# Performance work log

Hardware: AMD Instinct MI355X
Metric: run time of the kernel (lower is better)

Reference implementation:

```python
import jax, jax.numpy as jnp
import numpy as np
from jax import lax

EPS = 1e-5
NUM_CLASSES = 133


def conv2d(x, w, stride, pad, b=None):
    # x: [N,C,H,W], w: [O,I,kh,kw]
    out = lax.conv_general_dilated(x, w, (stride, stride), ((pad, pad), (pad, pad)),
                                   dimension_numbers=('NCHW', 'OIHW', 'NCHW'))
    if b is not None:
        out = out + b[None, :, None, None]
    return out


def cbn(x, y, embed_w, C):
    # ConditionalBatchNorm2d in training mode: batch stats (biased var), affine from embedding
    mean = x.mean(axis=(0, 2, 3), keepdims=True)
    var = x.var(axis=(0, 2, 3), keepdims=True)
    xn = (x - mean) * lax.rsqrt(var + EPS)
    gb = embed_w[y]                      # [O, 2C]
    gamma, beta = gb[:, :C], gb[:, C:]
    return gamma[:, :, None, None] * xn + beta[:, :, None, None]


def lrelu(x):
    return jnp.where(x >= 0, x, 0.2 * x)


def clstm_layer(x_seq, w, b, hidden_dim):
    # x_seq: [T, B, Cin, 16, 16] -> (all h: [T,B,hid,16,16], last h: [B,hid,16,16])
    B = x_seq.shape[1]
    h0 = jnp.zeros((B, hidden_dim, 16, 16), x_seq.dtype)

    def step(carry, x):
        h, c = carry
        cc = conv2d(jnp.concatenate([x, h], axis=1), w, 1, 2, b)  # k=5, pad=2
        i, f, o, g = jnp.split(cc, 4, axis=1)
        c = jax.nn.sigmoid(f) * c + jax.nn.sigmoid(i) * jnp.tanh(g)
        h = jax.nn.sigmoid(o) * jnp.tanh(c)
        return (h, c), h

    (h, _), hs = lax.scan(step, (h0, h0), x_seq)
    return hs, h


def setup_inputs() -> dict:
    key = jax.random.key(0)
    ks = jax.random.split(key, 24)
    O, C_in, H = 8, 512, 254
    B, T = 4, 2
    d = {}
    d['h'] = jax.random.normal(ks[0], (O, C_in, H, H), jnp.float32)
    d['objs'] = jax.random.randint(ks[1], (O,), 0, NUM_CLASSES)
    d['obj_to_img'] = jnp.repeat(jnp.arange(B), T)  # sorted, equal-sized groups

    def w(k, shape):
        fan_in = shape[1] * shape[2] * shape[3]
        return jax.random.normal(k, shape, jnp.float32) / np.sqrt(fan_in)

    def embed(k, C):
        g = 1.0 + 0.02 * jax.random.normal(k, (NUM_CLASSES, C), jnp.float32)
        return jnp.concatenate([g, jnp.zeros((NUM_CLASSES, C), jnp.float32)], axis=1)

    d['c1_w'] = w(ks[2], (32, 512, 1, 1))
    d['c2_w'] = w(ks[3], (64, 32, 4, 4))
    d['c3_w'] = w(ks[4], (128, 64, 4, 4))
    d['c4_w'] = w(ks[5], (256, 128, 4, 4))
    d['c5_w'] = w(ks[6], (512, 256, 4, 4))
    d['e1'] = embed(ks[7], 32)
    d['e2'] = embed(ks[8], 64)
    d['e3'] = embed(ks[9], 128)
    d['e4'] = embed(ks[10], 256)
    d['e5'] = embed(ks[11], 512)
    # ConvLSTM layers: hidden [128, 64, 64], kernel 5x5, input_dim 512
    d['lw0'] = w(ks[12], (4 * 128, 512 + 128, 5, 5))
    d['lb0'] = jnp.zeros((4 * 128,), jnp.float32)
    d['lw1'] = w(ks[13], (4 * 64, 128 + 64, 5, 5))
    d['lb1'] = jnp.zeros((4 * 64,), jnp.float32)
    d['lw2'] = w(ks[14], (4 * 64, 64 + 64, 5, 5))
    d['lb2'] = jnp.zeros((4 * 64,), jnp.float32)
    return d


def reference(objs, obj_to_img, h, c1_w, c2_w, c3_w, c4_w, c5_w,
              e1, e2, e3, e4, e5, lw0, lb0, lw1, lb1, lw2, lb2):
    x = lrelu(cbn(conv2d(h, c1_w, 1, 1), objs, e1, 32))    # [O,32,256,256]
    x = lrelu(cbn(conv2d(x, c2_w, 2, 1), objs, e2, 64))    # [O,64,128,128]
    x = lrelu(cbn(conv2d(x, c3_w, 2, 1), objs, e3, 128))   # [O,128,64,64]
    x = cbn(conv2d(x, c4_w, 2, 1), objs, e4, 256)          # no activation after bn4 (as in source)
    x = cbn(conv2d(x, c5_w, 2, 1), objs, e5, 512)          # [O,512,16,16], no activation after bn5

    # Group ragged per-image object sequences. The torch loop groups consecutive
    # equal obj_to_img ids; with equal group sizes this is a static reshape.
    o2i = np.asarray(obj_to_img)
    B = int(o2i.max()) + 1
    O = x.shape[0]
    T = O // B
    assert B * T == O, 'reference assumes equal-sized, sorted object groups'
    seq = x.reshape(B, T, 512, 16, 16).transpose(1, 0, 2, 3, 4)  # [T,B,512,16,16]

    hs, _ = clstm_layer(seq, lw0, lb0, 128)
    hs, _ = clstm_layer(hs, lw1, lb1, 64)
    _, h_last = clstm_layer(hs, lw2, lb2, 64)
    return h_last  # [B,64,16,16]
```

## Files before the change

kernel.cpp:

```cpp
#include <hip/hip_runtime.h>
#include <math.h>

#define LEAK 0.2f

typedef __attribute__((ext_vector_type(8))) short bf16x8;
typedef __attribute__((ext_vector_type(4))) float f32x4;

__device__ __forceinline__ unsigned short f2bf(float f) {
  unsigned u = __float_as_uint(f);
  u += 0x7FFFu + ((u >> 16) & 1u);
  return (unsigned short)(u >> 16);
}
__device__ __forceinline__ unsigned pack2(float a, float b) {
  return (unsigned)f2bf(a) | ((unsigned)f2bf(b) << 16);
}

#define MFMA16(a, b, c) __builtin_amdgcn_mfma_f32_16x16x32_bf16(a, b, c, 0, 0, 0)

__global__ __launch_bounds__(256) void wprepT_kernel(
    const float* c1w, const float* c2w, const float* c3w, const float* c4w,
    const float* c5w, const float* lw0, const float* lw1, const float* lw2,
    unsigned short* wb1, unsigned short* wb2, unsigned short* wb3,
    unsigned short* wb4, unsigned short* wb5, unsigned short* wbf0,
    unsigned short* wbf1, unsigned short* wbf2)
{
  __shared__ float lds[256 * 26];
  const int tid = threadIdx.x;
  int b = blockIdx.x;

  const float* src;
  unsigned short* dst;
  int T, OC, base;
  if (b < 8)         { src = c2w; dst = wb2;  T = 16; OC = 2048;   base = b * 256; }
  else if (b < 40)   { src = c3w; dst = wb3;  T = 16; OC = 8192;   base = (b - 8) * 256; }
  else if (b < 168)  { src = c4w; dst = wb4;  T = 16; OC = 32768;  base = (b - 40) * 256; }
  else if (b < 680)  { src = c5w; dst = wb5;  T = 16; OC = 131072; base = (b - 168) * 256; }
  else if (b < 872)  { src = lw1; dst = wbf1; T = 25; OC = 49152;  base = (b - 680) * 256; }
  else if (b < 1000) { src = lw2; dst = wbf2; T = 25; OC = 32768;  base = (b - 872) * 256; }
  else if (b < 2280) { src = lw0; dst = wbf0; T = 25; OC = 327680; base = (b - 1000) * 256; }
  else {
    int i = (b - 2280) * 256 + tid;
    int o = i >> 9, c = i & 511;
    wb1[(((c >> 5) * 32) + o) * 32 + (c & 31)] = f2bf(c1w[i]);
    return;
  }

  const float* sp = src + (size_t)base * T;
  for (int e = tid; e < 256 * T; e += 256) {
    int oc = e / T, tap = e - oc * T;
    lds[oc * 26 + tap] = sp[e];
  }
  __syncthreads();
  for (int tap = 0; tap < T; ++tap)
    dst[(size_t)tap * OC + base + tid] = f2bf(lds[tid * 26 + tap]);
}

__global__ __launch_bounds__(256) void conv1M_kernel(
    const float* __restrict__ h, const unsigned short* __restrict__ wbc,
    float* __restrict__ xT, float* __restrict__ part1)
{
  __shared__ __align__(16) unsigned short inT[512 * 40];
  __shared__ float red1[4][4][2][4][2];

  const int n = blockIdx.y;
  const int px0 = blockIdx.x * 512;
  const int tid = threadIdx.x, lane = tid & 63, wid = tid >> 6;
  const int ln15 = lane & 15, kg = lane >> 4;

  f32x4 acc[2][8];
#pragma unroll
  for (int m = 0; m < 2; ++m)
#pragma unroll
    for (int f = 0; f < 8; ++f) acc[m][f] = (f32x4){0.f, 0.f, 0.f, 0.f};

  for (int kc = 0; kc < 16; ++kc) {
    __syncthreads();
#pragma unroll
    for (int k = 0; k < 8; ++k) {
      const int u = tid + k * 256;
      const int chp = u >> 7;
      const int pxq = u & 127;
      const int ch = 2 * chp;
      const int pxl = 4 * pxq;
      const int pxg = px0 + pxl;
      const int r = pxg >> 8;
      const int c0 = pxg & 255;
      const bool rint = (r >= 1 && r <= 254);
      const float* hrow0 = h + ((size_t)(n * 512 + kc * 32 + ch)) * 64516
                             + (size_t)(r - 1) * 254 + (c0 - 1);
      const float* hrow1 = hrow0 + 64516;
      float v0[4], v1[4];
#pragma unroll
      for (int j = 0; j < 4; ++j) {
        const int c = c0 + j;
        const bool ok = rint && (c >= 1) && (c <= 254);
        v0[j] = ok ? hrow0[j] : 0.f;
        v1[j] = ok ? hrow1[j] : 0.f;
      }
      const int chs = ch ^ ((pxq & 3) << 3);
#pragma unroll
      for (int j = 0; j < 4; ++j)
        *(unsigned*)&inT[(pxl + j) * 40 + chs] = pack2(v0[j], v1[j]);
    }
    __syncthreads();

    const bf16x8 a0 = *(const bf16x8*)(wbc + ((size_t)(kc * 32 + ln15)) * 32 + kg * 8);
    const bf16x8 a1 = *(const bf16x8*)(wbc + ((size_t)(kc * 32 + 16 + ln15)) * 32 + kg * 8);
#pragma unroll
    for (int f = 0; f < 8; ++f) {
      const int pxr = wid * 128 + f * 16 + ln15;
      const int chs = (kg * 8) ^ (((pxr >> 2) & 3) << 3);
      const bf16x8 b = *(const bf16x8*)&inT[pxr * 40 + chs];
      acc[0][f] = MFMA16(a0, b, acc[0][f]);
      acc[1][f] = MFMA16(a1, b, acc[1][f]);
    }
  }

#pragma unroll
  for (int mf = 0; mf < 2; ++mf) {
#pragma unroll
    for (int f = 0; f < 8; ++f) {
      const int px = px0 + wid * 128 + f * 16 + ln15;
      const int o = mf * 16 + kg * 4;
      *(f32x4*)(xT + ((size_t)n * 65536 + px) * 32 + o) = acc[mf][f];
    }
  }

#pragma unroll
  for (int mf = 0; mf < 2; ++mf) {
#pragma unroll
    for (int j = 0; j < 4; ++j) {
      float s = 0.f, q = 0.f;
#pragma unroll
      for (int f = 0; f < 8; ++f) { float v = acc[mf][f][j]; s += v; q += v * v; }
#pragma unroll
      for (int mk = 1; mk < 16; mk <<= 1) {
        s += __shfl_xor(s, mk);
        q += __shfl_xor(q, mk);
      }
      if (ln15 == 0) { red1[wid][kg][mf][j][0] = s; red1[wid][kg][mf][j][1] = q; }
    }
  }
  __syncthreads();
  if (tid < 32) {
    const int mf = tid >> 4, kgi = (tid >> 2) & 3, j = tid & 3;
    float s = red1[0][kgi][mf][j][0] + red1[1][kgi][mf][j][0]
            + red1[2][kgi][mf][j][0] + red1[3][kgi][mf][j][0];
    float q = red1[0][kgi][mf][j][1] + red1[1][kgi][mf][j][1]
            + red1[2][kgi][mf][j][1] + red1[3][kgi][mf][j][1];
    atomicAdd(&part1[tid], s);
    atomicAdd(&part1[32 + tid], q);
  }
}

__global__ __launch_bounds__(256) void cbn1T_kernel(
    const float* __restrict__ xT, const float* __restrict__ part1, float invN,
    const float* __restrict__ e1, const int* __restrict__ objs,
    unsigned short* __restrict__ T2)
{
  __shared__ float st[32][4];
  const int n = blockIdx.y;
  if (threadIdx.x < 32) {
    int y = objs[n];
    float s = part1[threadIdx.x], q = part1[32 + threadIdx.x];
    float mean = s * invN;
    st[threadIdx.x][0] = mean;
    st[threadIdx.x][1] = rsqrtf(q * invN - mean * mean + 1e-5f);
    st[threadIdx.x][2] = e1[(size_t)y * 64 + threadIdx.x];
    st[threadIdx.x][3] = e1[(size_t)y * 64 + 32 + threadIdx.x];
  }
  __syncthreads();
  const int pix = blockIdx.x * 256 + threadIdx.x;
  const int r = pix >> 8, c = pix & 255;
  const float* src = xT + ((size_t)n * 65536 + pix) * 32;
  unsigned short* dst = T2 + ((size_t)n * 66564 + (size_t)(r + 1) * 258 + (c + 1)) * 32;
  unsigned outw[16];
#pragma unroll
  for (int q = 0; q < 8; ++q) {
    float4 t = ((const float4*)src)[q];
    float v[4] = {t.x, t.y, t.z, t.w};
#pragma unroll
    for (int j = 0; j < 4; ++j) {
      int ch = q * 4 + j;
      float z = (v[j] - st[ch][0]) * st[ch][1] * st[ch][2] + st[ch][3];
      v[j] = z >= 0.f ? z : LEAK * z;
    }
    outw[2 * q]     = pack2(v[0], v[1]);
    outw[2 * q + 1] = pack2(v[2], v[3]);
  }
  uint4* d4 = (uint4*)dst;
#pragma unroll
  for (int q = 0; q < 4; ++q)
    d4[q] = make_uint4(outw[4*q], outw[4*q+1], outw[4*q+2], outw[4*q+3]);
}

template <int C, int O, int H, int WM>
__global__ __launch_bounds__(256) void conv4T_kernel(
    const unsigned short* __restrict__ Tin, const unsigned short* __restrict__ wb,
    float* __restrict__ raw, float* __restrict__ part)
{
  constexpr int HIN2 = 2 * H + 2;
  constexpr int KC = C / 32;
  constexpr int WN4 = 4 / WM;
  constexpr int NT = WM;
  constexpr int LOGH = (H == 128 ? 7 : (H == 64 ? 6 : (H == 32 ? 5 : 4)));
  __shared__ float red[4][4][2][4][2];
  const int o0 = blockIdx.x * (WM * 32);
  const int strip = blockIdx.y;
  const int n = blockIdx.z;
  const int tid = threadIdx.x, lane = tid & 63, wid = tid >> 6;
  const int wm = wid / WN4, wn = wid % WN4;
  const int ln15 = lane & 15, kg = lane >> 4;
  const unsigned short* inb = Tin + (size_t)n * (HIN2 * HIN2) * C;

  f32x4 acc[2][NT];
#pragma unroll
  for (int m = 0; m < 2; ++m)
#pragma unroll
    for (int nt = 0; nt < NT; ++nt) acc[m][nt] = (f32x4){0.f, 0.f, 0.f, 0.f};

  int r_[NT], c_[NT];
#pragma unroll
  for (int nt = 0; nt < NT; ++nt) {
    const int gp = strip * 64 + (wn * NT + nt) * 16;
    r_[nt] = gp >> LOGH;
    c_[nt] = (gp & (H - 1)) + ln15;
  }

  for (int kc = 0; kc < KC; ++kc) {
    const int cb = kc * 32 + kg * 8;
#pragma unroll
    for (int tap = 0; tap < 16; ++tap) {
      const int ky = tap >> 2, kx = tap & 3;
      const unsigned short* ap = wb + ((size_t)tap * O + o0 + wm * 32 + ln15) * C + cb;
      bf16x8 a0 = *(const bf16x8*)ap;
      bf16x8 a1 = *(const bf16x8*)(ap + (size_t)16 * C);
#pragma unroll
      for (int nt = 0; nt < NT; ++nt) {
        bf16x8 b = *(const bf16x8*)(inb + (size_t)((2 * r_[nt] + ky) * HIN2 + 2 * c_[nt] + kx) * C + cb);
        acc[0][nt] = MFMA16(a0, b, acc[0][nt]);
        acc[1][nt] = MFMA16(a1, b, acc[1][nt]);
      }
    }
  }

#pragma unroll
  for (int mf = 0; mf < 2; ++mf) {
    const int o = o0 + wm * 32 + mf * 16 + kg * 4;
#pragma unroll
    for (int nt = 0; nt < NT; ++nt) {
      const int gp = strip * 64 + (wn * NT + nt) * 16 + ln15;
      *(f32x4*)(raw + ((size_t)n * (H * H) + gp) * O + o) = acc[mf][nt];
    }
  }

#pragma unroll
  for (int mf = 0; mf < 2; ++mf) {
#pragma unroll
    for (int j = 0; j < 4; ++j) {
      float s = 0.f, q = 0.f;
#pragma unroll
      for (int nt = 0; nt < NT; ++nt) { float v = acc[mf][nt][j]; s += v; q += v * v; }
#pragma unroll
      for (int mk = 1; mk < 16; mk <<= 1) {
        s += __shfl_xor(s, mk);
        q += __shfl_xor(q, mk);
      }
      if (ln15 == 0) { red[wid][kg][mf][j][0] = s; red[wid][kg][mf][j][1] = q; }
    }
  }
  __syncthreads();
  if (tid < WM * 32) {
    const int wmi = tid >> 5, mf = (tid >> 4) & 1, kgi = (tid >> 2) & 3, j = tid & 3;
    float s = 0.f, q = 0.f;
#pragma unroll
    for (int w = 0; w < WN4; ++w) {
      s += red[wmi * WN4 + w][kgi][mf][j][0];
      q += red[wmi * WN4 + w][kgi][mf][j][1];
    }
    atomicAdd(&part[o0 + tid], s);
    atomicAdd(&part[O + o0 + tid], q);
  }
}

template <int C, int H, int P2, int CSO, bool LRELU, bool LMAP>
__global__ __launch_bounds__(256) void cbnT_kernel(
    const float* __restrict__ raw, const float* __restrict__ part, float invN,
    const float* __restrict__ embed, const int* __restrict__ objs,
    unsigned short* __restrict__ Tout)
{
  constexpr int W2 = H + 2 * P2;
  constexpr int LOGH = (H == 128 ? 7 : (H == 64 ? 6 : (H == 32 ? 5 : 4)));
  const int n = blockIdx.y;
  const int y = objs[n];
  const int pix = blockIdx.x * 64 + (threadIdx.x >> 2);
  const int r = pix >> LOGH, c = pix & (H - 1);
  const float* src = raw + ((size_t)n * (H * H) + pix) * C;
  const size_t nb = LMAP ? (size_t)((n & 1) * 4 + (n >> 1)) * (W2 * W2) * CSO
                         : (size_t)n * (W2 * W2) * CSO;
  unsigned short* dst = Tout + nb + ((size_t)(r + P2) * W2 + c + P2) * CSO;
  const float* gam = embed + (size_t)y * 2 * C;
  const float* bet = gam + C;
  for (int cs = (threadIdx.x & 3); cs < C / 8; cs += 4) {
    float4 ps0 = ((const float4*)part)[cs * 2],       ps1 = ((const float4*)part)[cs * 2 + 1];
    float4 pq0 = ((const float4*)(part + C))[cs * 2], pq1 = ((const float4*)(part + C))[cs * 2 + 1];
    float4 g0 = ((const float4*)gam)[cs * 2], g1 = ((const float4*)gam)[cs * 2 + 1];
    float4 b0 = ((const float4*)bet)[cs * 2], b1 = ((const float4*)bet)[cs * 2 + 1];
    float4 v0 = ((const float4*)src)[cs * 2], v1 = ((const float4*)src)[cs * 2 + 1];
    float sv[8] = {ps0.x, ps0.y, ps0.z, ps0.w, ps1.x, ps1.y, ps1.z, ps1.w};
    float qv[8] = {pq0.x, pq0.y, pq0.z, pq0.w, pq1.x, pq1.y, pq1.z, pq1.w};
    float gv[8] = {g0.x, g0.y, g0.z, g0.w, g1.x, g1.y, g1.z, g1.w};
    float bv[8] = {b0.x, b0.y, b0.z, b0.w, b1.x, b1.y, b1.z, b1.w};
    float vv[8] = {v0.x, v0.y, v0.z, v0.w, v1.x, v1.y, v1.z, v1.w};
    float o_[8];
#pragma unroll
    for (int k = 0; k < 8; ++k) {
      float m = sv[k] * invN;
      float rs = rsqrtf(qv[k] * invN - m * m + 1e-5f);
      float z = (vv[k] - m) * rs * gv[k] + bv[k];
      o_[k] = (LRELU && z < 0.f) ? LEAK * z : z;
    }
    ((uint4*)dst)[cs] = make_uint4(pack2(o_[0], o_[1]), pack2(o_[2], o_[3]),
                                   pack2(o_[4], o_[5]), pack2(o_[6], o_[7]));
  }
}

template <int O, int CS, int WM, int WN>
__global__ __launch_bounds__(256) void conv5L_kernel(
    const unsigned short* __restrict__ Lin, const unsigned short* __restrict__ wbf,
    float* __restrict__ pp, int kbeg, int slot0, size_t lin_tstr, size_t pp_tstr)
{
  constexpr int FN = 16 / WN;
  const int o0 = blockIdx.x * (WM * 32);
  const int b = blockIdx.y & 3, t = blockIdx.y >> 2;
  const int ks = blockIdx.z;
  const int tid = threadIdx.x, lane = tid & 63, wid = tid >> 6;
  const int wm = wid / WN, wn = wid % WN;
  const int ln15 = lane & 15, kg = lane >> 4;
  const unsigned short* inb = Lin + (size_t)t * lin_tstr + (size_t)b * 400 * CS;
  float* ppb = pp + (size_t)t * pp_tstr + ((size_t)(slot0 + ks) * 4 + b) * (256 * O);

  f32x4 acc[2][FN];
#pragma unroll
  for (int m = 0; m < 2; ++m)
#pragma unroll
    for (int nt = 0; nt < FN; ++nt) acc[m][nt] = (f32x4){0.f, 0.f, 0.f, 0.f};

  const int cb = (kbeg + ks) * 32 + kg * 8;
  for (int tap = 0; tap < 25; ++tap) {
    const int ty = tap / 5, tx = tap - 5 * ty;
    const unsigned short* ap = wbf + ((size_t)tap * O + o0 + wm * 32 + ln15) * CS + cb;
    bf16x8 a0 = *(const bf16x8*)ap;
    bf16x8 a1 = *(const bf16x8*)(ap + (size_t)16 * CS);
#pragma unroll
    for (int nt = 0; nt < FN; ++nt) {
      const int p = (wn * FN + nt) * 16 + ln15;
      const int prow = p >> 4, pcol = p & 15;
      bf16x8 bfv = *(const bf16x8*)(inb + (size_t)((prow + ty) * 20 + pcol + tx) * CS + cb);
      acc[0][nt] = MFMA16(a0, bfv, acc[0][nt]);
      acc[1][nt] = MFMA16(a1, bfv, acc[1][nt]);
    }
  }

#pragma unroll
  for (int mf = 0; mf < 2; ++mf) {
    const int o = o0 + wm * 32 + mf * 16 + kg * 4;
#pragma unroll
    for (int nt = 0; nt < FN; ++nt) {
      const int pix = (wn * FN + nt) * 16 + ln15;
      *(f32x4*)(ppb + (size_t)pix * O + o) = acc[mf][nt];
    }
  }
}

template <int Hc, int CS, int CX, int CSN>
__global__ __launch_bounds__(256) void lstm_pointT_kernel(
    const float* __restrict__ pp, int KS, const float* __restrict__ bias,
    float* __restrict__ cT, unsigned short* __restrict__ own,
    unsigned short* __restrict__ nxt, float* __restrict__ fout)
{
  constexpr int C4 = Hc / 4;
  constexpr int O = 4 * Hc;
  constexpr int LOGC4 = (C4 == 32 ? 5 : 4);
  const int i = blockIdx.x * 256 + threadIdx.x;
  const int c4 = i & (C4 - 1);
  const int pix = (i >> LOGC4) & 255;
  const int b = i >> (LOGC4 + 8);

  float g[4][4];
#pragma unroll
  for (int gt = 0; gt < 4; ++gt)
#pragma unroll
    for (int j = 0; j < 4; ++j) g[gt][j] = 0.f;

  for (int ks = 0; ks < KS; ++ks) {
    const float* base = pp + (((size_t)(ks * 4 + b)) * 256 + pix) * O + c4 * 4;
#pragma unroll
    for (int gt = 0; gt < 4; ++gt) {
      float4 v = *(const float4*)(base + gt * Hc);
      g[gt][0] += v.x; g[gt][1] += v.y; g[gt][2] += v.z; g[gt][3] += v.w;
    }
  }
#pragma unroll
  for (int gt = 0; gt < 4; ++gt) {
    float4 bv = *(const float4*)(bias + gt * Hc + c4 * 4);
    g[gt][0] += bv.x; g[gt][1] += bv.y; g[gt][2] += bv.z; g[gt][3] += bv.w;
  }

  float* cp = cT + ((size_t)b * 256 + pix) * Hc + c4 * 4;
  float4 cold = *(const float4*)cp;
  float co[4] = {cold.x, cold.y, cold.z, cold.w};
  float hn[4];
#pragma unroll
  for (int j = 0; j < 4; ++j) {
    float si = 1.f / (1.f + expf(-g[0][j]));
    float sf = 1.f / (1.f + expf(-g[1][j]));
    float so = 1.f / (1.f + expf(-g[2][j]));
    float cn = sf * co[j] + si * tanhf(g[3][j]);
    co[j] = cn;
    hn[j] = so * tanhf(cn);
  }
  *(float4*)cp = make_float4(co[0], co[1], co[2], co[3]);

  const int prow = pix >> 4, pcol = pix & 15;
  const int ppix = (prow + 2) * 20 + pcol + 2;
  uint2 hb = make_uint2(pack2(hn[0], hn[1]), pack2(hn[2], hn[3]));
  if (own) *(uint2*)(own + ((size_t)b * 400 + ppix) * CS + CX + c4 * 4) = hb;
  if (nxt) *(uint2*)(nxt + ((size_t)b * 400 + ppix) * CSN + c4 * 4) = hb;
  if (fout) {
#pragma unroll
    for (int j = 0; j < 4; ++j)
      fout[((size_t)b * Hc + c4 * 4 + j) * 256 + pix] = hn[j];
  }
}

extern "C" void kernel_launch(void* const* d_in, const int* in_sizes, int n_in,
                              void* d_out, int out_size, void* d_ws, size_t ws_size,
                              hipStream_t stream)
{
  const float* h    = (const float*)d_in[0];
  const int*   objs = (const int*)  d_in[1];
  const float* c1w  = (const float*)d_in[3];
  const float* c2w  = (const float*)d_in[4];
  const float* c3w  = (const float*)d_in[5];
  const float* c4w  = (const float*)d_in[6];
  const float* c5w  = (const float*)d_in[7];
  const float* e1   = (const float*)d_in[8];
  const float* e2   = (const float*)d_in[9];
  const float* e3   = (const float*)d_in[10];
  const float* e4   = (const float*)d_in[11];
  const float* e5   = (const float*)d_in[12];
  const float* lw0  = (const float*)d_in[13];
  const float* lb0  = (const float*)d_in[14];
  const float* lw1  = (const float*)d_in[15];
  const float* lb1  = (const float*)d_in[16];
  const float* lw2  = (const float*)d_in[17];
  const float* lb2  = (const float*)d_in[18];

  char* p = (char*)d_ws;
  auto alloc = [&](size_t bytes) { char* r = p; p += (bytes + 255) & ~(size_t)255; return r; };
  float* x1T  = (float*)alloc((size_t)8 * 65536 * 32 * 4);
  float* raw2 = (float*)alloc((size_t)8 * 16384 * 64 * 4);
  float* raw3 = (float*)alloc((size_t)8 * 4096 * 128 * 4);
  float* raw4 = (float*)alloc((size_t)8 * 1024 * 256 * 4);
  float* raw5 = (float*)alloc((size_t)8 * 256 * 512 * 4);
  float* pp   = (float*)alloc((size_t)2 * 20 * 4 * 256 * 512 * 4);
  unsigned short* wb1  = (unsigned short*)alloc((size_t)32 * 512 * 2);
  unsigned short* wb2  = (unsigned short*)alloc((size_t)16 * 64 * 32 * 2);
  unsigned short* wb3  = (unsigned short*)alloc((size_t)16 * 128 * 64 * 2);
  unsigned short* wb4  = (unsigned short*)alloc((size_t)16 * 256 * 128 * 2);
  unsigned short* wb5  = (unsigned short*)alloc((size_t)16 * 512 * 256 * 2);
  unsigned short* wbf0 = (unsigned short*)alloc((size_t)25 * 512 * 640 * 2);
  unsigned short* wbf1 = (unsigned short*)alloc((size_t)25 * 256 * 192 * 2);
  unsigned short* wbf2 = (unsigned short*)alloc((size_t)25 * 256 * 128 * 2);
  char* zbase = p;
  unsigned short* T2 = (unsigned short*)alloc((size_t)8 * 66564 * 32 * 2);
  unsigned short* T3 = (unsigned short*)alloc((size_t)8 * 16900 * 64 * 2);
  unsigned short* T4 = (unsigned short*)alloc((size_t)8 * 4356 * 128 * 2);
  unsigned short* T5 = (unsigned short*)alloc((size_t)8 * 1156 * 256 * 2);
  unsigned short* L0in = (unsigned short*)alloc((size_t)2 * 4 * 400 * 640 * 2);
  unsigned short* L1in = (unsigned short*)alloc((size_t)2 * 4 * 400 * 192 * 2);
  unsigned short* L2in = (unsigned short*)alloc((size_t)2 * 4 * 400 * 128 * 2);
  float* cT0 = (float*)alloc((size_t)4 * 256 * 128 * 4);
  float* cT1 = (float*)alloc((size_t)4 * 256 * 64 * 4);
  float* cT2 = (float*)alloc((size_t)4 * 256 * 64 * 4);
  float* part1 = (float*)alloc(2 * 32 * 4);
  float* part2 = (float*)alloc(2 * 64 * 4);
  float* part3 = (float*)alloc(2 * 128 * 4);
  float* part4 = (float*)alloc(2 * 256 * 4);
  float* part5 = (float*)alloc(2 * 512 * 4);
  size_t zsize = (size_t)(p - zbase);

  hipMemsetAsync(zbase, 0, zsize, stream);
  wprepT_kernel<<<2344, 256, 0, stream>>>(
      c1w, c2w, c3w, c4w, c5w, lw0, lw1, lw2,
      wb1, wb2, wb3, wb4, wb5, wbf0, wbf1, wbf2);

  conv1M_kernel<<<dim3(128, 8), 256, 0, stream>>>(h, wb1, x1T, part1);
  cbn1T_kernel<<<dim3(256, 8), 256, 0, stream>>>(x1T, part1, 1.f / (float)(8 * 65536), e1, objs, T2);

  conv4T_kernel<32, 64, 128, 2><<<dim3(1, 256, 8), 256, 0, stream>>>(T2, wb2, raw2, part2);
  cbnT_kernel<64, 128, 1, 64, true, false><<<dim3(256, 8), 256, 0, stream>>>(
      raw2, part2, 1.f / (float)(8 * 16384), e2, objs, T3);

  conv4T_kernel<64, 128, 64, 2><<<dim3(2, 64, 8), 256, 0, stream>>>(T3, wb3, raw3, part3);
  cbnT_kernel<128, 64, 1, 128, true, false><<<dim3(64, 8), 256, 0, stream>>>(
      raw3, part3, 1.f / (float)(8 * 4096), e3, objs, T4);

  conv4T_kernel<128, 256, 32, 1><<<dim3(8, 16, 8), 256, 0, stream>>>(T4, wb4, raw4, part4);
  cbnT_kernel<256, 32, 1, 256, false, false><<<dim3(16, 8), 256, 0, stream>>>(
      raw4, part4, 1.f / (float)(8 * 1024), e4, objs, T5);

  conv4T_kernel<256, 512, 16, 1><<<dim3(16, 4, 8), 256, 0, stream>>>(T5, wb5, raw5, part5);
  cbnT_kernel<512, 16, 2, 640, false, true><<<dim3(4, 8), 256, 0, stream>>>(
      raw5, part5, 1.f / (float)(8 * 256), e5, objs, L0in);

  {
    const size_t LINT = (size_t)4 * 400 * 640;
    const size_t PPT  = (size_t)20 * 4 * 256 * 512;
    conv5L_kernel<512, 640, 2, 2><<<dim3(8, 8, 16), 256, 0, stream>>>(
        L0in, wbf0, pp, 0, 0, LINT, PPT);
    lstm_pointT_kernel<128, 640, 512, 192><<<128, 256, 0, stream>>>(
        pp, 16, lb0, cT0, L0in + LINT, L1in, nullptr);
    conv5L_kernel<512, 640, 2, 2><<<dim3(8, 4, 4), 256, 0, stream>>>(
        L0in + LINT, wbf0, pp + PPT, 16, 16, 0, 0);
    lstm_pointT_kernel<128, 640, 512, 192><<<128, 256, 0, stream>>>(
        pp + PPT, 20, lb0, cT0, nullptr, L1in + (size_t)4 * 400 * 192, nullptr);
  }

  {
    const size_t LINT = (size_t)4 * 400 * 192;
    const size_t PPT  = (size_t)6 * 4 * 256 * 256;
    conv5L_kernel<256, 192, 1, 4><<<dim3(8, 8, 4), 256, 0, stream>>>(
        L1in, wbf1, pp, 0, 0, LINT, PPT);
    lstm_pointT_kernel<64, 192, 128, 128><<<64, 256, 0, stream>>>(
        pp, 4, lb1, cT1, L1in + LINT, L2in, nullptr);
    conv5L_kernel<256, 192, 1, 4><<<dim3(8, 4, 2), 256, 0, stream>>>(
        L1in + LINT, wbf1, pp + PPT, 4, 4, 0, 0);
    lstm_pointT_kernel<64, 192, 128, 128><<<64, 256, 0, stream>>>(
        pp + PPT, 6, lb1, cT1, nullptr, L2in + (size_t)4 * 400 * 128, nullptr);
  }

  {
    const size_t LINT = (size_t)4 * 400 * 128;
    const size_t PPT  = (size_t)4 * 4 * 256 * 256;
    conv5L_kernel<256, 128, 1, 4><<<dim3(8, 8, 2), 256, 0, stream>>>(
        L2in, wbf2, pp, 0, 0, LINT, PPT);
    lstm_pointT_kernel<64, 128, 64, 1><<<64, 256, 0, stream>>>(
        pp, 2, lb2, cT2, L2in + LINT, nullptr, nullptr);
    conv5L_kernel<256, 128, 1, 4><<<dim3(8, 4, 2), 256, 0, stream>>>(
        L2in + LINT, wbf2, pp + PPT, 2, 2, 0, 0);
    lstm_pointT_kernel<64, 128, 64, 1><<<64, 256, 0, stream>>>(
        pp + PPT, 4, lb2, cT2, nullptr, nullptr, (float*)d_out);
  }
}
```

Baseline: 1.041 ms.

## Fuse ConvLSTM stage kernels into one persistent kernel with grid barriers

Replaces the twelve ConvLSTM conv and pointwise launches with a single persistent 256-block kernel. Phases are separated by an atomic-counter grid barrier, and work units are mapped onto block indices inside each phase. The aim is to remove per-launch overhead and inter-kernel gaps in the small, latency-bound recurrent section. The risks are barrier spin cost, idle blocks in the smaller phases, and reliance on all 256 blocks being co-resident to avoid deadlock.

```diff
diff --git a/kernel.cpp b/kernel.cpp
--- a/kernel.cpp
+++ b/kernel.cpp
@@ -326,14 +326,13 @@
 }
 
 template <int O, int CS, int WM, int WN>
-__global__ __launch_bounds__(256) void conv5L_kernel(
+__device__ __forceinline__ void conv5L_unit(
+    int bx, int b, int t, int ks,
     const unsigned short* __restrict__ Lin, const unsigned short* __restrict__ wbf,
     float* __restrict__ pp, int kbeg, int slot0, size_t lin_tstr, size_t pp_tstr)
 {
   constexpr int FN = 16 / WN;
-  const int o0 = blockIdx.x * (WM * 32);
-  const int b = blockIdx.y & 3, t = blockIdx.y >> 2;
-  const int ks = blockIdx.z;
+  const int o0 = bx * (WM * 32);
   const int tid = threadIdx.x, lane = tid & 63, wid = tid >> 6;
   const int wm = wid / WN, wn = wid % WN;
   const int ln15 = lane & 15, kg = lane >> 4;
@@ -374,15 +373,14 @@
 }
 
 template <int Hc, int CS, int CX, int CSN>
-__global__ __launch_bounds__(256) void lstm_pointT_kernel(
-    const float* __restrict__ pp, int KS, const float* __restrict__ bias,
-    float* __restrict__ cT, unsigned short* __restrict__ own,
-    unsigned short* __restrict__ nxt, float* __restrict__ fout)
+__device__ __forceinline__ void lstm_point_unit(
+    int u, const float* __restrict__ pp, int KS, const float* __restrict__ bias,
+    float* __restrict__ cT, unsigned short* own, unsigned short* nxt, float* fout)
 {
   constexpr int C4 = Hc / 4;
   constexpr int O = 4 * Hc;
   constexpr int LOGC4 = (C4 == 32 ? 5 : 4);
-  const int i = blockIdx.x * 256 + threadIdx.x;
+  const int i = u * 256 + threadIdx.x;
   const int c4 = i & (C4 - 1);
   const int pix = (i >> LOGC4) & 255;
   const int b = i >> (LOGC4 + 8);
@@ -432,6 +430,86 @@
     for (int j = 0; j < 4; ++j)
       fout[((size_t)b * Hc + c4 * 4 + j) * 256 + pix] = hn[j];
   }
+}
+
+__device__ __forceinline__ void gbar(unsigned* cnt, unsigned target) {
+  __syncthreads();
+  if (threadIdx.x == 0) {
+    __threadfence();
+    atomicAdd(cnt, 1u);
+    while (atomicAdd(cnt, 0u) < target)
+      __builtin_amdgcn_s_sleep(8);
+    __threadfence();
+  }
+  __syncthreads();
+}
+
+__global__ __launch_bounds__(256) void lstm_persist_kernel(
+    unsigned short* L0in, unsigned short* L1in, unsigned short* L2in,
+    const unsigned short* __restrict__ wbf0, const unsigned short* __restrict__ wbf1,
+    const unsigned short* __restrict__ wbf2,
+    const float* __restrict__ lb0, const float* __restrict__ lb1,
+    const float* __restrict__ lb2,
+    float* cT0, float* cT1, float* cT2,
+    float* pp, float* dout, unsigned* bar)
+{
+  const int blk = blockIdx.x;
+  const size_t LINT0 = (size_t)4 * 400 * 640, PPT0 = (size_t)20 * 4 * 256 * 512;
+  const size_t LINT1 = (size_t)4 * 400 * 192, PPT1 = (size_t)6 * 4 * 256 * 256;
+  const size_t LINT2 = (size_t)4 * 400 * 128, PPT2 = (size_t)4 * 4 * 256 * 256;
+  unsigned tgt = 0;
+
+#pragma unroll
+  for (int j = 0; j < 4; ++j) {
+    const int u = blk + 256 * j;
+    const int bx = u & 7, byy = (u >> 3) & 7, ks = u >> 6;
+    conv5L_unit<512, 640, 2, 2>(bx, byy & 3, byy >> 2, ks, L0in, wbf0, pp, 0, 0, LINT0, PPT0);
+  }
+  tgt += 256; gbar(bar, tgt);
+  if (blk < 128)
+    lstm_point_unit<128, 640, 512, 192>(blk, pp, 16, lb0, cT0, L0in + LINT0, L1in, nullptr);
+  tgt += 256; gbar(bar, tgt);
+  if (blk < 128) {
+    const int bx = blk & 7, b = (blk >> 3) & 3, ks = blk >> 5;
+    conv5L_unit<512, 640, 2, 2>(bx, b, 0, ks, L0in + LINT0, wbf0, pp + PPT0, 16, 16, 0, 0);
+  }
+  tgt += 256; gbar(bar, tgt);
+  if (blk < 128)
+    lstm_point_unit<128, 640, 512, 192>(blk, pp + PPT0, 20, lb0, cT0, nullptr,
+                                        L1in + LINT1, nullptr);
+  tgt += 256; gbar(bar, tgt);
+  {
+    const int bx = blk & 7, byy = (blk >> 3) & 7, ks = blk >> 6;
+    conv5L_unit<256, 192, 1, 4>(bx, byy & 3, byy >> 2, ks, L1in, wbf1, pp, 0, 0, LINT1, PPT1);
+  }
+  tgt += 256; gbar(bar, tgt);
+  if (blk < 64)
+    lstm_point_unit<64, 192, 128, 128>(blk, pp, 4, lb1, cT1, L1in + LINT1, L2in, nullptr);
+  tgt += 256; gbar(bar, tgt);
+  if (blk < 64) {
+    const int bx = blk & 7, b = (blk >> 3) & 3, ks = blk >> 5;
+    conv5L_unit<256, 192, 1, 4>(bx, b, 0, ks, L1in + LINT1, wbf1, pp + PPT1, 4, 4, 0, 0);
+  }
+  tgt += 256; gbar(bar, tgt);
+  if (blk < 64)
+    lstm_point_unit<64, 192, 128, 128>(blk, pp + PPT1, 6, lb1, cT1, nullptr,
+                                       L2in + LINT2, nullptr);
+  tgt += 256; gbar(bar, tgt);
+  if (blk < 128) {
+    const int bx = blk & 7, byy = (blk >> 3) & 7, ks = blk >> 6;
+    conv5L_unit<256, 128, 1, 4>(bx, byy & 3, byy >> 2, ks, L2in, wbf2, pp, 0, 0, LINT2, PPT2);
+  }
+  tgt += 256; gbar(bar, tgt);
+  if (blk < 64)
+    lstm_point_unit<64, 128, 64, 1>(blk, pp, 2, lb2, cT2, L2in + LINT2, nullptr, nullptr);
+  tgt += 256; gbar(bar, tgt);
+  if (blk < 64) {
+    const int bx = blk & 7, b = (blk >> 3) & 3, ks = blk >> 5;
+    conv5L_unit<256, 128, 1, 4>(bx, b, 0, ks, L2in + LINT2, wbf2, pp + PPT2, 2, 2, 0, 0);
+  }
+  tgt += 256; gbar(bar, tgt);
+  if (blk < 64)
+    lstm_point_unit<64, 128, 64, 1>(blk, pp + PPT2, 4, lb2, cT2, nullptr, nullptr, dout);
 }
 
 extern "C" void kernel_launch(void* const* d_in, const int* in_sizes, int n_in,
@@ -489,6 +567,7 @@
   float* part3 = (float*)alloc(2 * 128 * 4);
   float* part4 = (float*)alloc(2 * 256 * 4);
   float* part5 = (float*)alloc(2 * 512 * 4);
+  unsigned* bar = (unsigned*)alloc(256);
   size_t zsize = (size_t)(p - zbase);
 
   hipMemsetAsync(zbase, 0, zsize, stream);
@@ -515,42 +594,7 @@
   cbnT_kernel<512, 16, 2, 640, false, true><<<dim3(4, 8), 256, 0, stream>>>(
       raw5, part5, 1.f / (float)(8 * 256), e5, objs, L0in);
 
-  {
-    const size_t LINT = (size_t)4 * 400 * 640;
-    const size_t PPT  = (size_t)20 * 4 * 256 * 512;
-    conv5L_kernel<512, 640, 2, 2><<<dim3(8, 8, 16), 256, 0, stream>>>(
-        L0in, wbf0, pp, 0, 0, LINT, PPT);
-    lstm_pointT_kernel<128, 640, 512, 192><<<128, 256, 0, stream>>>(
-        pp, 16, lb0, cT0, L0in + LINT, L1in, nullptr);
-    conv5L_kernel<512, 640, 2, 2><<<dim3(8, 4, 4), 256, 0, stream>>>(
-        L0in + LINT, wbf0, pp + PPT, 16, 16, 0, 0);
-    lstm_pointT_kernel<128, 640, 512, 192><<<128, 256, 0, stream>>>(
-        pp + PPT, 20, lb0, cT0, nullptr, L1in + (size_t)4 * 400 * 192, nullptr);
-  }
-
-  {
-    const size_t LINT = (size_t)4 * 400 * 192;
-    const size_t PPT  = (size_t)6 * 4 * 256 * 256;
-    conv5L_kernel<256, 192, 1, 4><<<dim3(8, 8, 4), 256, 0, stream>>>(
-        L1in, wbf1, pp, 0, 0, LINT, PPT);
-    lstm_pointT_kernel<64, 192, 128, 128><<<64, 256, 0, stream>>>(
-        pp, 4, lb1, cT1, L1in + LINT, L2in, nullptr);
-    conv5L_kernel<256, 192, 1, 4><<<dim3(8, 4, 2), 256, 0, stream>>>(
-        L1in + LINT, wbf1, pp + PPT, 4, 4, 0, 0);
-    lstm_pointT_kernel<64, 192, 128, 128><<<64, 256, 0, stream>>>(
-        pp + PPT, 6, lb1, cT1, nullptr, L2in + (size_t)4 * 400 * 128, nullptr);
-  }
-
-  {
-    const size_t LINT = (size_t)4 * 400 * 128;
-    const size_t PPT  = (size_t)4 * 4 * 256 * 256;
-    conv5L_kernel<256, 128, 1, 4><<<dim3(8, 8, 2), 256, 0, stream>>>(
-        L2in, wbf2, pp, 0, 0, LINT, PPT);
-    lstm_pointT_kernel<64, 128, 64, 1><<<64, 256, 0, stream>>>(
-        pp, 2, lb2, cT2, L2in + LINT, nullptr, nullptr);
-    conv5L_kernel<256, 128, 1, 4><<<dim3(8, 4, 2), 256, 0, stream>>>(
-        L2in + LINT, wbf2, pp + PPT, 2, 2, 0, 0);
-    lstm_pointT_kernel<64, 128, 64, 1><<<64, 256, 0, stream>>>(
-        pp + PPT, 4, lb2, cT2, nullptr, nullptr, (float*)d_out);
-  }
-}
+  lstm_persist_kernel<<<256, 256, 0, stream>>>(
+      L0in, L1in, L2in, wbf0, wbf1, wbf2, lb0, lb1, lb2,
+      cT0, cT1, cT2, pp, (float*)d_out, bar);
+}
```

Result: slower. 1.234 ms (+18.5%).
